# Performance work log

Hardware: AMD Instinct MI355X
Metric: run time of the kernel (lower is better)

Reference implementation:

```python
import jax, jax.numpy as jnp
import numpy as np

B, T, C = 2, 4096, 512
H = 8
MEMORY = 256  # window: key j visible to query i iff 0 <= i - j <= MEMORY


def setup_inputs() -> dict:
    key = jax.random.key(0)
    k1, k2, k3 = jax.random.split(key, 3)
    x = jax.random.normal(k1, (B, T, C), dtype=jnp.float32)
    w_attn = jax.random.normal(k2, (3 * C, C), dtype=jnp.float32) * 0.02
    w_proj = jax.random.normal(k3, (C, C), dtype=jnp.float32) * 0.02
    return {"x": x, "w_attn": w_attn, "w_proj": w_proj}


def reference(x, w_attn, w_proj):
    b, t, c = x.shape
    d = c // H
    # fused QKV projection (Linear without bias): x @ W^T
    qkv = jnp.einsum('btc,fc->btf', x, w_attn)  # [B,T,3C]
    q, k, v = jnp.split(qkv, 3, axis=-1)
    # [B,T,C] -> [B,H,T,d]
    q = q.reshape(b, t, H, d).transpose(0, 2, 1, 3)
    k = k.reshape(b, t, H, d).transpose(0, 2, 1, 3)
    v = v.reshape(b, t, H, d).transpose(0, 2, 1, 3)
    # sliding-window causal mask: tril(0) & ~tril(-memory-1)
    i = jnp.arange(t)[:, None]
    j = jnp.arange(t)[None, :]
    mask = (j <= i) & (i - j <= MEMORY)  # [T,T] bool
    scores = jnp.einsum('bhqd,bhkd->bhqk', q, k) * (1.0 / np.sqrt(d))
    scores = jnp.where(mask, scores, -jnp.inf)
    attn = jax.nn.softmax(scores, axis=-1)
    y = jnp.einsum('bhqk,bhkd->bhqd', attn, v)  # [B,H,T,d]
    y = y.transpose(0, 2, 1, 3).reshape(b, t, c)
    # output projection
    y = jnp.einsum('btc,fc->btf', y, w_proj)
    return y
```

## Files before the change

kernel.cpp:

```cpp
#include <hip/hip_runtime.h>
#include <hip/hip_bf16.h>
#include <stdint.h>

#define BB 2
#define TT 4096
#define CC 512
#define HH 8
#define MEM 256

typedef unsigned short u16;
typedef __bf16 bf16x8 __attribute__((ext_vector_type(8)));
typedef float floatx4 __attribute__((ext_vector_type(4)));

__device__ inline u16 f2bf(float f) {
  uint32_t u = __float_as_uint(f);
  uint32_t r = (u + 0x7fffu + ((u >> 16) & 1u)) >> 16;
  return (u16)r;
}
__device__ inline u16 f2bf_r(float f) {
  return (u16)((__float_as_uint(f) + 0x8000u) >> 16);
}

__device__ inline void gld16(const u16* g, u16* lds) {
  __builtin_amdgcn_global_load_lds(
      (const __attribute__((address_space(1))) uint32_t*)g,
      (__attribute__((address_space(3))) uint32_t*)lds, 16, 0, 0);
}

__global__ __launch_bounds__(256) void cvt_all(const float* __restrict__ x,
                                               const float* __restrict__ wa,
                                               const float* __restrict__ wp,
                                               u16* __restrict__ xb,
                                               u16* __restrict__ wab,
                                               u16* __restrict__ wpb) {
  int i = blockIdx.x * 256 + threadIdx.x;
  const float* s; u16* d; int off;
  if (i < 1048576) { s = x; d = xb; off = i; }
  else if (i < 1245184) { s = wa; d = wab; off = i - 1048576; }
  else { s = wp; d = wpb; off = i - 1245184; }
  float4 v = *reinterpret_cast<const float4*>(s + (size_t)off * 4);
  ushort4 o;
  o.x = f2bf(v.x); o.y = f2bf(v.y); o.z = f2bf(v.z); o.w = f2bf(v.w);
  *reinterpret_cast<ushort4*>(d + (size_t)off * 4) = o;
}

template <bool OUT_F32>
__global__ __launch_bounds__(256) void gemm_bt(const u16* __restrict__ A,
                                               const u16* __restrict__ Bw,
                                               void* __restrict__ Cout,
                                               int M, int N, int K) {
  __shared__ __align__(16) u16 As[128 * 32];
  __shared__ __align__(16) u16 Bs[128 * 32];
  const int tid = threadIdx.x;
  const int w = tid >> 6, lane = tid & 63, quad = lane >> 4, l16 = lane & 15;
  const int wm = w >> 1, wn = w & 1;
  const int m0 = blockIdx.x * 128, n0 = blockIdx.y * 128;

  floatx4 acc[4][4] = {};
  const int nK = K >> 5;
  for (int kb = 0; kb < nK; ++kb) {
    const int kof = kb * 32;
    {
      int c = tid;
      gld16(A + (size_t)(m0 + (c >> 2)) * K + kof + (c & 3) * 8, As + (size_t)c * 8);
      c = tid + 256;
      gld16(A + (size_t)(m0 + (c >> 2)) * K + kof + (c & 3) * 8, As + (size_t)c * 8);
      c = tid;
      gld16(Bw + (size_t)(n0 + (c >> 2)) * K + kof + (c & 3) * 8, Bs + (size_t)c * 8);
      c = tid + 256;
      gld16(Bw + (size_t)(n0 + (c >> 2)) * K + kof + (c & 3) * 8, Bs + (size_t)c * 8);
    }
    __syncthreads();
    bf16x8 af[4], bfr[4];
#pragma unroll
    for (int i = 0; i < 4; i++)
      af[i] = *reinterpret_cast<const bf16x8*>(&As[(wm * 64 + i * 16 + l16) * 32 + quad * 8]);
#pragma unroll
    for (int i = 0; i < 4; i++)
      bfr[i] = *reinterpret_cast<const bf16x8*>(&Bs[(wn * 64 + i * 16 + l16) * 32 + quad * 8]);
#pragma unroll
    for (int mi = 0; mi < 4; mi++)
#pragma unroll
      for (int ni = 0; ni < 4; ni++)
        acc[mi][ni] = __builtin_amdgcn_mfma_f32_16x16x32_bf16(af[mi], bfr[ni], acc[mi][ni], 0, 0, 0);
    __syncthreads();
  }
#pragma unroll
  for (int mi = 0; mi < 4; mi++) {
    int row = m0 + wm * 64 + mi * 16 + quad * 4;
#pragma unroll
    for (int ni = 0; ni < 4; ni++) {
      int col = n0 + wn * 64 + ni * 16 + l16;
#pragma unroll
      for (int r = 0; r < 4; r++) {
        if (OUT_F32)
          ((float*)Cout)[(size_t)(row + r) * N + col] = acc[mi][ni][r];
        else
          ((u16*)Cout)[(size_t)(row + r) * N + col] = f2bf(acc[mi][ni][r]);
      }
    }
  }
}

__global__ __launch_bounds__(256) void gemm_bt_n64(const u16* __restrict__ A,
                                                   const u16* __restrict__ Bw,
                                                   float* __restrict__ C,
                                                   int M, int N, int K) {
  __shared__ __align__(16) u16 As[128 * 32];
  __shared__ __align__(16) u16 Bs[64 * 32];
  const int tid = threadIdx.x;
  const int w = tid >> 6, lane = tid & 63, quad = lane >> 4, l16 = lane & 15;
  const int m0 = blockIdx.x * 128, n0 = blockIdx.y * 64;

  floatx4 acc[2][4] = {};
  const int nK = K >> 5;
  for (int kb = 0; kb < nK; ++kb) {
    const int kof = kb * 32;
    {
      int c = tid;
      gld16(A + (size_t)(m0 + (c >> 2)) * K + kof + (c & 3) * 8, As + (size_t)c * 8);
      c = tid + 256;
      gld16(A + (size_t)(m0 + (c >> 2)) * K + kof + (c & 3) * 8, As + (size_t)c * 8);
      c = tid;
      gld16(Bw + (size_t)(n0 + (c >> 2)) * K + kof + (c & 3) * 8, Bs + (size_t)c * 8);
    }
    __syncthreads();
    bf16x8 af[2], bfr[4];
#pragma unroll
    for (int i = 0; i < 2; i++)
      af[i] = *reinterpret_cast<const bf16x8*>(&As[(w * 32 + i * 16 + l16) * 32 + quad * 8]);
#pragma unroll
    for (int i = 0; i < 4; i++)
      bfr[i] = *reinterpret_cast<const bf16x8*>(&Bs[(i * 16 + l16) * 32 + quad * 8]);
#pragma unroll
    for (int mi = 0; mi < 2; mi++)
#pragma unroll
      for (int ni = 0; ni < 4; ni++)
        acc[mi][ni] = __builtin_amdgcn_mfma_f32_16x16x32_bf16(af[mi], bfr[ni], acc[mi][ni], 0, 0, 0);
    __syncthreads();
  }
#pragma unroll
  for (int mi = 0; mi < 2; mi++) {
    int row = m0 + w * 32 + mi * 16 + quad * 4;
#pragma unroll
    for (int ni = 0; ni < 4; ni++) {
      int col = n0 + ni * 16 + l16;
#pragma unroll
      for (int r = 0; r < 4; r++)
        C[(size_t)(row + r) * N + col] = acc[mi][ni][r];
    }
  }
}

__global__ __launch_bounds__(256) void attn_win(const u16* __restrict__ qkv,
                                                u16* __restrict__ y) {
  const int q0 = blockIdx.x * 64;
  const int h = blockIdx.y;
  const int b = blockIdx.z;
  const int tid = threadIdx.x;
  const int w = tid >> 6, lane = tid & 63, quad = lane >> 4, l16 = lane & 15;

  __shared__ __align__(16) u16 Qs[64 * 64];
  __shared__ __align__(16) u16 Ks[64 * 64];
  __shared__ __align__(16) u16 Vt[64 * 72];
  __shared__ __align__(16) u16 Ps[4][16 * 72];

  const size_t baseQ = ((size_t)(b * TT + q0)) * 1536 + h * 64;
  {
    int c = tid, row = c >> 3, blk = (c & 7) ^ (row & 7);
    gld16(qkv + baseQ + (size_t)row * 1536 + blk * 8, Qs + (size_t)c * 8);
    c = tid + 256; row = c >> 3; blk = (c & 7) ^ (row & 7);
    gld16(qkv + baseQ + (size_t)row * 1536 + blk * 8, Qs + (size_t)c * 8);
  }
  __syncthreads();
  const int qrow = w * 16 + l16;
  bf16x8 qf0 = *reinterpret_cast<const bf16x8*>(&Qs[qrow * 64 + (quad ^ (l16 & 7)) * 8]);
  bf16x8 qf1 = *reinterpret_cast<const bf16x8*>(&Qs[qrow * 64 + ((quad + 4) ^ (l16 & 7)) * 8]);
#pragma unroll
  for (int e = 0; e < 8; e++) {
    qf0[e] = qf0[e] * (__bf16)0.125f;
    qf1[e] = qf1[e] * (__bf16)0.125f;
  }

  floatx4 acc_o[4] = {};
  float l_acc[4] = {0.f, 0.f, 0.f, 0.f};

  const int s_min = (q0 >= 256) ? 0 : ((256 - q0) >> 6);
  for (int s = s_min; s < 5; ++s) {
    const int k0 = q0 - 256 + s * 64;
    const size_t baseK = ((size_t)(b * TT + k0)) * 1536 + 512 + h * 64;
    {
      int c = tid, row = c >> 3, blk = (c & 7) ^ (row & 7);
      gld16(qkv + baseK + (size_t)row * 1536 + blk * 8, Ks + (size_t)c * 8);
      c = tid + 256; row = c >> 3; blk = (c & 7) ^ (row & 7);
      gld16(qkv + baseK + (size_t)row * 1536 + blk * 8, Ks + (size_t)c * 8);
    }
    const size_t baseV = ((size_t)(b * TT + k0)) * 1536 + 1024 + h * 64;
#pragma unroll
    for (int half = 0; half < 2; ++half) {
      int c = tid + half * 256;
      int key = c >> 3, dc = c & 7;
      u16 tmp[8];
      *reinterpret_cast<uint4*>(tmp) =
          *reinterpret_cast<const uint4*>(qkv + baseV + (size_t)key * 1536 + dc * 8);
      int col = key ^ (dc * 8);
#pragma unroll
      for (int e = 0; e < 8; e++) Vt[(dc * 8 + e) * 72 + col] = tmp[e];
    }
    __syncthreads();

    floatx4 sc[4] = {};
#pragma unroll
    for (int nt = 0; nt < 4; nt++) {
      int krow = nt * 16 + l16;
      bf16x8 b0 = *reinterpret_cast<const bf16x8*>(&Ks[krow * 64 + (quad ^ (l16 & 7)) * 8]);
      bf16x8 b1 = *reinterpret_cast<const bf16x8*>(&Ks[krow * 64 + ((quad + 4) ^ (l16 & 7)) * 8]);
      sc[nt] = __builtin_amdgcn_mfma_f32_16x16x32_bf16(qf0, b0, sc[nt], 0, 0, 0);
      sc[nt] = __builtin_amdgcn_mfma_f32_16x16x32_bf16(qf1, b1, sc[nt], 0, 0, 0);
    }
    if (s == 4) {
#pragma unroll
      for (int nt = 0; nt < 4; nt++)
#pragma unroll
        for (int r = 0; r < 4; r++)
          if (w * 16 + quad * 4 + r < nt * 16 + l16) sc[nt][r] = -1e30f;
    } else if (s == 0) {
#pragma unroll
      for (int nt = 0; nt < 4; nt++)
#pragma unroll
        for (int r = 0; r < 4; r++)
          if (w * 16 + quad * 4 + r > nt * 16 + l16) sc[nt][r] = -1e30f;
    }
#pragma unroll
    for (int nt = 0; nt < 4; nt++) {
#pragma unroll
      for (int r = 0; r < 4; r++) {
        float p = __expf(sc[nt][r] - 4.0f);
        l_acc[r] += p;
        Ps[w][(quad * 4 + r) * 72 + nt * 16 + l16] = f2bf_r(p);
      }
    }
#pragma unroll
    for (int ki = 0; ki < 2; ki++) {
      bf16x8 pf = *reinterpret_cast<const bf16x8*>(&Ps[w][l16 * 72 + ki * 32 + quad * 8]);
#pragma unroll
      for (int nt = 0; nt < 4; nt++) {
        int d = nt * 16 + l16;
        bf16x8 vf = *reinterpret_cast<const bf16x8*>(
            &Vt[d * 72 + ((ki * 32 + quad * 8) ^ (d & 56))]);
        acc_o[nt] = __builtin_amdgcn_mfma_f32_16x16x32_bf16(pf, vf, acc_o[nt], 0, 0, 0);
      }
    }
    __syncthreads();
  }
#pragma unroll
  for (int r = 0; r < 4; r++) {
    float l = l_acc[r];
    l += __shfl_xor(l, 1);
    l += __shfl_xor(l, 2);
    l += __shfl_xor(l, 4);
    l += __shfl_xor(l, 8);
    float inv = 1.f / l;
    int row = q0 + w * 16 + quad * 4 + r;
    size_t base = (size_t)(b * TT + row) * 512 + h * 64;
#pragma unroll
    for (int nt = 0; nt < 4; nt++)
      y[base + nt * 16 + l16] = f2bf(acc_o[nt][r] * inv);
  }
}

extern "C" void kernel_launch(void* const* d_in, const int* in_sizes, int n_in,
                              void* d_out, int out_size, void* d_ws, size_t ws_size,
                              hipStream_t stream) {
  const float* x = (const float*)d_in[0];
  const float* w_attn = (const float*)d_in[1];
  const float* w_proj = (const float*)d_in[2];
  float* out = (float*)d_out;

  u16* xb = (u16*)d_ws;
  u16* wab = xb + (size_t)8192 * 512;
  u16* wpb = wab + (size_t)1536 * 512;
  u16* qkv = wpb + (size_t)512 * 512;
  u16* yb = qkv + (size_t)8192 * 1536;

  cvt_all<<<5120, 256, 0, stream>>>(x, w_attn, w_proj, xb, wab, wpb);
  gemm_bt<false><<<dim3(64, 12), 256, 0, stream>>>(xb, wab, (void*)qkv, 8192, 1536, 512);
  attn_win<<<dim3(TT / 64, HH, BB), 256, 0, stream>>>(qkv, yb);
  gemm_bt_n64<<<dim3(64, 8), 256, 0, stream>>>(yb, wpb, out, 8192, 512, 512);
}
```

Baseline: 125.6 us.

## Enlarge attention query tile to 128 rows and prefetch V one step ahead

The windowed attention kernel now processes 128 queries per block, with each wave handling 32 rows. Each loaded K/V tile therefore serves twice as many queries, which cuts redundant K/V global traffic. V for the next key block is loaded into registers while the current one is transposed into LDS, and per-wave masking modes skip fully masked tiles at the window edges. The cost is more registers per thread and half as many blocks (512), which lowers parallelism on a large GPU.

New measurement: 124.1 us. Within noise of the previous version (-1.1%).

```diff
diff --git a/kernel.cpp b/kernel.cpp
--- a/kernel.cpp
+++ b/kernel.cpp
@@ -152,41 +152,54 @@
   }
 }
 
-__global__ __launch_bounds__(256) void attn_win(const u16* __restrict__ qkv,
-                                                u16* __restrict__ y) {
-  const int q0 = blockIdx.x * 64;
+__global__ __launch_bounds__(256, 2) void attn_win(const u16* __restrict__ qkv,
+                                                   u16* __restrict__ y) {
+  const int q0 = blockIdx.x * 128;
   const int h = blockIdx.y;
   const int b = blockIdx.z;
   const int tid = threadIdx.x;
   const int w = tid >> 6, lane = tid & 63, quad = lane >> 4, l16 = lane & 15;
 
-  __shared__ __align__(16) u16 Qs[64 * 64];
+  __shared__ __align__(16) u16 Qs[128 * 64];
   __shared__ __align__(16) u16 Ks[64 * 64];
   __shared__ __align__(16) u16 Vt[64 * 72];
-  __shared__ __align__(16) u16 Ps[4][16 * 72];
+  __shared__ __align__(16) u16 Ps[4][32 * 72];
 
   const size_t baseQ = ((size_t)(b * TT + q0)) * 1536 + h * 64;
+#pragma unroll
+  for (int j = 0; j < 4; j++) {
+    int c = tid + j * 256, row = c >> 3, blk = (c & 7) ^ (row & 7);
+    gld16(qkv + baseQ + (size_t)row * 1536 + blk * 8, Qs + (size_t)c * 8);
+  }
+  __syncthreads();
+  bf16x8 qf[2][2];
+#pragma unroll
+  for (int mi = 0; mi < 2; mi++) {
+    int row = w * 32 + mi * 16 + l16;
+    qf[mi][0] = *reinterpret_cast<const bf16x8*>(&Qs[row * 64 + (quad ^ (l16 & 7)) * 8]);
+    qf[mi][1] = *reinterpret_cast<const bf16x8*>(&Qs[row * 64 + ((quad + 4) ^ (l16 & 7)) * 8]);
+#pragma unroll
+    for (int e = 0; e < 8; e++) {
+      qf[mi][0][e] = qf[mi][0][e] * (__bf16)0.125f;
+      qf[mi][1][e] = qf[mi][1][e] * (__bf16)0.125f;
+    }
+  }
+
+  floatx4 acc_o[2][4] = {};
+  float l_acc[2][4] = {{0.f, 0.f, 0.f, 0.f}, {0.f, 0.f, 0.f, 0.f}};
+
+  const int s_min = (q0 >= 256) ? 0 : ((256 - q0) >> 6);
+  const int key_v = tid >> 3, dc_v = tid & 7;
+  const int key_v1 = (tid + 256) >> 3, dc_v1 = tid & 7;
+
+  uint4 vp0, vp1;
   {
-    int c = tid, row = c >> 3, blk = (c & 7) ^ (row & 7);
-    gld16(qkv + baseQ + (size_t)row * 1536 + blk * 8, Qs + (size_t)c * 8);
-    c = tid + 256; row = c >> 3; blk = (c & 7) ^ (row & 7);
-    gld16(qkv + baseQ + (size_t)row * 1536 + blk * 8, Qs + (size_t)c * 8);
-  }
-  __syncthreads();
-  const int qrow = w * 16 + l16;
-  bf16x8 qf0 = *reinterpret_cast<const bf16x8*>(&Qs[qrow * 64 + (quad ^ (l16 & 7)) * 8]);
-  bf16x8 qf1 = *reinterpret_cast<const bf16x8*>(&Qs[qrow * 64 + ((quad + 4) ^ (l16 & 7)) * 8]);
-#pragma unroll
-  for (int e = 0; e < 8; e++) {
-    qf0[e] = qf0[e] * (__bf16)0.125f;
-    qf1[e] = qf1[e] * (__bf16)0.125f;
-  }
-
-  floatx4 acc_o[4] = {};
-  float l_acc[4] = {0.f, 0.f, 0.f, 0.f};
-
-  const int s_min = (q0 >= 256) ? 0 : ((256 - q0) >> 6);
-  for (int s = s_min; s < 5; ++s) {
+    size_t baseV = ((size_t)(b * TT + (q0 - 256 + s_min * 64))) * 1536 + 1024 + h * 64;
+    vp0 = *reinterpret_cast<const uint4*>(qkv + baseV + (size_t)key_v * 1536 + dc_v * 8);
+    vp1 = *reinterpret_cast<const uint4*>(qkv + baseV + (size_t)key_v1 * 1536 + dc_v1 * 8);
+  }
+
+  for (int s = s_min; s < 6; ++s) {
     const int k0 = q0 - 256 + s * 64;
     const size_t baseK = ((size_t)(b * TT + k0)) * 1536 + 512 + h * 64;
     {
@@ -195,78 +208,107 @@
       c = tid + 256; row = c >> 3; blk = (c & 7) ^ (row & 7);
       gld16(qkv + baseK + (size_t)row * 1536 + blk * 8, Ks + (size_t)c * 8);
     }
-    const size_t baseV = ((size_t)(b * TT + k0)) * 1536 + 1024 + h * 64;
-#pragma unroll
-    for (int half = 0; half < 2; ++half) {
-      int c = tid + half * 256;
-      int key = c >> 3, dc = c & 7;
+    {
       u16 tmp[8];
-      *reinterpret_cast<uint4*>(tmp) =
-          *reinterpret_cast<const uint4*>(qkv + baseV + (size_t)key * 1536 + dc * 8);
-      int col = key ^ (dc * 8);
-#pragma unroll
-      for (int e = 0; e < 8; e++) Vt[(dc * 8 + e) * 72 + col] = tmp[e];
-    }
-    __syncthreads();
-
-    floatx4 sc[4] = {};
-#pragma unroll
-    for (int nt = 0; nt < 4; nt++) {
-      int krow = nt * 16 + l16;
-      bf16x8 b0 = *reinterpret_cast<const bf16x8*>(&Ks[krow * 64 + (quad ^ (l16 & 7)) * 8]);
-      bf16x8 b1 = *reinterpret_cast<const bf16x8*>(&Ks[krow * 64 + ((quad + 4) ^ (l16 & 7)) * 8]);
-      sc[nt] = __builtin_amdgcn_mfma_f32_16x16x32_bf16(qf0, b0, sc[nt], 0, 0, 0);
-      sc[nt] = __builtin_amdgcn_mfma_f32_16x16x32_bf16(qf1, b1, sc[nt], 0, 0, 0);
-    }
-    if (s == 4) {
+      *reinterpret_cast<uint4*>(tmp) = vp0;
+      int col = key_v ^ (dc_v * 8);
+#pragma unroll
+      for (int e = 0; e < 8; e++) Vt[(dc_v * 8 + e) * 72 + col] = tmp[e];
+      *reinterpret_cast<uint4*>(tmp) = vp1;
+      col = key_v1 ^ (dc_v1 * 8);
+#pragma unroll
+      for (int e = 0; e < 8; e++) Vt[(dc_v1 * 8 + e) * 72 + col] = tmp[e];
+    }
+    if (s < 5) {
+      size_t baseV = ((size_t)(b * TT + k0 + 64)) * 1536 + 1024 + h * 64;
+      vp0 = *reinterpret_cast<const uint4*>(qkv + baseV + (size_t)key_v * 1536 + dc_v * 8);
+      vp1 = *reinterpret_cast<const uint4*>(qkv + baseV + (size_t)key_v1 * 1536 + dc_v1 * 8);
+    }
+    __syncthreads();
+
+    int mode = 0;
+    if (s == 0) mode = (w < 2) ? 1 : 3;
+    else if (s == 1) mode = (w < 2) ? 0 : 1;
+    else if (s == 4) mode = (w < 2) ? 2 : 0;
+    else if (s == 5) mode = (w < 2) ? 3 : 2;
+
+    if (mode != 3) {
+      bf16x8 bfr[4][2];
+#pragma unroll
+      for (int nt = 0; nt < 4; nt++) {
+        int krow = nt * 16 + l16;
+        bfr[nt][0] = *reinterpret_cast<const bf16x8*>(&Ks[krow * 64 + (quad ^ (l16 & 7)) * 8]);
+        bfr[nt][1] = *reinterpret_cast<const bf16x8*>(&Ks[krow * 64 + ((quad + 4) ^ (l16 & 7)) * 8]);
+      }
+      floatx4 sc[2][4] = {};
+#pragma unroll
+      for (int mi = 0; mi < 2; mi++)
+#pragma unroll
+        for (int nt = 0; nt < 4; nt++) {
+          sc[mi][nt] = __builtin_amdgcn_mfma_f32_16x16x32_bf16(qf[mi][0], bfr[nt][0], sc[mi][nt], 0, 0, 0);
+          sc[mi][nt] = __builtin_amdgcn_mfma_f32_16x16x32_bf16(qf[mi][1], bfr[nt][1], sc[mi][nt], 0, 0, 0);
+        }
+      const int hqb = (w & 1) * 32 + quad * 4;
+      if (mode == 1) {
+#pragma unroll
+        for (int mi = 0; mi < 2; mi++)
+#pragma unroll
+          for (int nt = 0; nt < 4; nt++)
+#pragma unroll
+            for (int r = 0; r < 4; r++)
+              if (hqb + mi * 16 + r > nt * 16 + l16) sc[mi][nt][r] = -1e30f;
+      } else if (mode == 2) {
+#pragma unroll
+        for (int mi = 0; mi < 2; mi++)
+#pragma unroll
+          for (int nt = 0; nt < 4; nt++)
+#pragma unroll
+            for (int r = 0; r < 4; r++)
+              if (hqb + mi * 16 + r < nt * 16 + l16) sc[mi][nt][r] = -1e30f;
+      }
+#pragma unroll
+      for (int mi = 0; mi < 2; mi++)
+#pragma unroll
+        for (int nt = 0; nt < 4; nt++)
+#pragma unroll
+          for (int r = 0; r < 4; r++) {
+            float p = __expf(sc[mi][nt][r] - 4.0f);
+            l_acc[mi][r] += p;
+            Ps[w][(mi * 16 + quad * 4 + r) * 72 + nt * 16 + l16] = f2bf_r(p);
+          }
+#pragma unroll
+      for (int mi = 0; mi < 2; mi++)
+#pragma unroll
+        for (int ki = 0; ki < 2; ki++) {
+          bf16x8 pf = *reinterpret_cast<const bf16x8*>(
+              &Ps[w][(mi * 16 + l16) * 72 + ki * 32 + quad * 8]);
+#pragma unroll
+          for (int nt = 0; nt < 4; nt++) {
+            int d = nt * 16 + l16;
+            bf16x8 vf = *reinterpret_cast<const bf16x8*>(
+                &Vt[d * 72 + ((ki * 32 + quad * 8) ^ (d & 56))]);
+            acc_o[mi][nt] = __builtin_amdgcn_mfma_f32_16x16x32_bf16(pf, vf, acc_o[mi][nt], 0, 0, 0);
+          }
+        }
+    }
+    __syncthreads();
+  }
+#pragma unroll
+  for (int mi = 0; mi < 2; mi++)
+#pragma unroll
+    for (int r = 0; r < 4; r++) {
+      float l = l_acc[mi][r];
+      l += __shfl_xor(l, 1);
+      l += __shfl_xor(l, 2);
+      l += __shfl_xor(l, 4);
+      l += __shfl_xor(l, 8);
+      float inv = 1.f / l;
+      int row = q0 + w * 32 + mi * 16 + quad * 4 + r;
+      size_t base = (size_t)(b * TT + row) * 512 + h * 64;
 #pragma unroll
       for (int nt = 0; nt < 4; nt++)
-#pragma unroll
-        for (int r = 0; r < 4; r++)
-          if (w * 16 + quad * 4 + r < nt * 16 + l16) sc[nt][r] = -1e30f;
-    } else if (s == 0) {
-#pragma unroll
-      for (int nt = 0; nt < 4; nt++)
-#pragma unroll
-        for (int r = 0; r < 4; r++)
-          if (w * 16 + quad * 4 + r > nt * 16 + l16) sc[nt][r] = -1e30f;
-    }
-#pragma unroll
-    for (int nt = 0; nt < 4; nt++) {
-#pragma unroll
-      for (int r = 0; r < 4; r++) {
-        float p = __expf(sc[nt][r] - 4.0f);
-        l_acc[r] += p;
-        Ps[w][(quad * 4 + r) * 72 + nt * 16 + l16] = f2bf_r(p);
-      }
-    }
-#pragma unroll
-    for (int ki = 0; ki < 2; ki++) {
-      bf16x8 pf = *reinterpret_cast<const bf16x8*>(&Ps[w][l16 * 72 + ki * 32 + quad * 8]);
-#pragma unroll
-      for (int nt = 0; nt < 4; nt++) {
-        int d = nt * 16 + l16;
-        bf16x8 vf = *reinterpret_cast<const bf16x8*>(
-            &Vt[d * 72 + ((ki * 32 + quad * 8) ^ (d & 56))]);
-        acc_o[nt] = __builtin_amdgcn_mfma_f32_16x16x32_bf16(pf, vf, acc_o[nt], 0, 0, 0);
-      }
-    }
-    __syncthreads();
-  }
-#pragma unroll
-  for (int r = 0; r < 4; r++) {
-    float l = l_acc[r];
-    l += __shfl_xor(l, 1);
-    l += __shfl_xor(l, 2);
-    l += __shfl_xor(l, 4);
-    l += __shfl_xor(l, 8);
-    float inv = 1.f / l;
-    int row = q0 + w * 16 + quad * 4 + r;
-    size_t base = (size_t)(b * TT + row) * 512 + h * 64;
-#pragma unroll
-    for (int nt = 0; nt < 4; nt++)
-      y[base + nt * 16 + l16] = f2bf(acc_o[nt][r] * inv);
-  }
+        y[base + nt * 16 + l16] = f2bf(acc_o[mi][nt][r] * inv);
+    }
 }
 
 extern "C" void kernel_launch(void* const* d_in, const int* in_sizes, int n_in,
@@ -285,6 +327,6 @@
 
   cvt_all<<<5120, 256, 0, stream>>>(x, w_attn, w_proj, xb, wab, wpb);
   gemm_bt<false><<<dim3(64, 12), 256, 0, stream>>>(xb, wab, (void*)qkv, 8192, 1536, 512);
-  attn_win<<<dim3(TT / 64, HH, BB), 256, 0, stream>>>(qkv, yb);
+  attn_win<<<dim3(TT / 128, HH, BB), 256, 0, stream>>>(qkv, yb);
   gemm_bt_n64<<<dim3(64, 8), 256, 0, stream>>>(yb, wpb, out, 8192, 512, 512);
 }
```
